# Performance work log

Measured on AMD Instinct MI355X. Metric: run time of the kernel, lower is better.

The kernel has to match this reference:

```python
import jax, jax.numpy as jnp
import numpy as np

NUM_HEADS = 16
INACTIVE = 4          # cfg_comp.attention_heads_inactive
SIG_DIM = 64          # cfg_comp.attention_heads_signature_dim
MLP_HIDDEN = 512      # cfg_comp.attention_heads_inference_mlp_hidden


def setup_inputs() -> dict:
    key = jax.random.key(0)
    ks = jax.random.split(key, 16)
    S, B, E = 2048, 2, 1024
    def xavier(k, shape, gain=1.0):
        fan_in, fan_out = shape[1], shape[0]
        a = gain * np.sqrt(6.0 / (fan_in + fan_out))
        return jax.random.uniform(k, shape, jnp.float32, -a, a)
    g = 1.0 / np.sqrt(2.0)
    return {
        "query": jax.random.normal(ks[0], (S, B, E), jnp.float32),
        "q_w": xavier(ks[1], (E, E), g), "q_b": jnp.zeros((E,), jnp.float32),
        "k_w": xavier(ks[2], (E, E), g), "k_b": jnp.zeros((E,), jnp.float32),
        "v_w": xavier(ks[3], (E, E), g), "v_b": jnp.zeros((E,), jnp.float32),
        "out_w": xavier(ks[4], (E, E)), "out_b": jnp.zeros((E,), jnp.float32),
        "inf1_w": xavier(ks[5], (MLP_HIDDEN, E), np.sqrt(2.0)),
        "inf1_b": jnp.zeros((MLP_HIDDEN,), jnp.float32),
        "inf2_w": xavier(ks[6], (SIG_DIM, MLP_HIDDEN), np.sqrt(2.0)),
        "inf2_b": jnp.zeros((SIG_DIM,), jnp.float32),
        "head_sig": jax.random.normal(ks[7], (NUM_HEADS, SIG_DIM), jnp.float32)
                    * np.sqrt(2.0 / (NUM_HEADS + SIG_DIM)),
    }


def _head_mask(query, inf1_w, inf1_b, inf2_w, inf2_b, head_sig):
    # inference_masking_step: (S, B, E) -> binary mask (B, H, S)
    t = jax.nn.relu(query @ inf1_w.T + inf1_b)          # (S, B, hidden)
    t = t @ inf2_w.T + inf2_b                            # (S, B, sig)
    s = t @ head_sig.T                                   # (S, B, H) head scores
    keep = NUM_HEADS - INACTIVE
    kth = jax.lax.top_k(s, keep)[0][..., -1]             # (S, B) kth-largest score
    mask = (s >= kth[..., None]).astype(query.dtype)     # 1 at top-`keep` heads
    mask = jax.lax.stop_gradient(mask)                   # scatter of constants in torch
    return jnp.transpose(mask, (1, 2, 0))                # (B, H, S)


def reference(query, q_w, q_b, k_w, k_b, v_w, v_b, out_w, out_b,
              inf1_w, inf1_b, inf2_w, inf2_b, head_sig):
    S, B, E = query.shape
    H, D = NUM_HEADS, E // NUM_HEADS
    scaling = D ** (-0.5)

    q = (query @ q_w.T + q_b) * scaling                  # (S, B, E)
    k = query @ k_w.T + k_b
    v = query @ v_w.T + v_b
    # (S, B, E) -> (B, H, S, D)
    to_bhsd = lambda x: jnp.transpose(x.reshape(S, B, H, D), (1, 2, 0, 3))
    q, k, v = to_bhsd(q), to_bhsd(k), to_bhsd(v)

    attn = jax.nn.softmax(jnp.einsum("bhqd,bhkd->bhqk", q, k), axis=-1)
    o = jnp.einsum("bhqk,bhkd->bhqd", attn, v)           # (B, H, S, D)

    mask = _head_mask(query, inf1_w, inf1_b, inf2_w, inf2_b, head_sig)  # (B, H, S)
    o = o * mask[..., None]                              # gate per head per position

    out = jnp.transpose(o, (2, 0, 1, 3)).reshape(S, B, E)
    return out @ out_w.T + out_b
```

## Files before the change

### kernel.cpp

```cpp
#include <hip/hip_runtime.h>
#include <hip/hip_bf16.h>

#define S_LEN 2048
#define BATCH 2
#define EDIM 1024
#define NHEAD 16
#define DHEAD 64
#define HIDDEN 512
#define SIGD 64
#define KEEP 12

typedef __attribute__((ext_vector_type(8))) short bf16x8;
typedef __attribute__((ext_vector_type(4))) float f32x4;

static __device__ __forceinline__ float bf2f(short s) {
  unsigned int u = ((unsigned int)(unsigned short)s) << 16;
  float f; __builtin_memcpy(&f, &u, 4); return f;
}
static __device__ __forceinline__ short f2bf(float f) {
  unsigned int u; __builtin_memcpy(&u, &f, 4);
  u += 0x7fffu + ((u >> 16) & 1u);
  return (short)(u >> 16);
}

#if __has_builtin(__builtin_amdgcn_exp2f)
static __device__ __forceinline__ float fexp2(float x) { return __builtin_amdgcn_exp2f(x); }
#else
static __device__ __forceinline__ float fexp2(float x) { return exp2f(x); }
#endif

static __device__ __forceinline__ void gl_lds16(const short* g, short* l) {
  __builtin_amdgcn_global_load_lds(
      (const __attribute__((address_space(1))) unsigned int*)g,
      (__attribute__((address_space(3))) unsigned int*)l, 16, 0, 0);
}

static __device__ __forceinline__ float bperm_f(int idx, float v) {
  return __builtin_bit_cast(float,
      __builtin_amdgcn_ds_bpermute(idx, __builtin_bit_cast(int, v)));
}

__global__ __launch_bounds__(256) void cvt_all(
    const float* __restrict__ query, const float* __restrict__ inf1_w,
    const float* __restrict__ qw, const float* __restrict__ kw,
    const float* __restrict__ vw, const float* __restrict__ ow,
    short* __restrict__ qh, short* __restrict__ ql,
    short* __restrict__ w1h, short* __restrict__ w1l,
    short* __restrict__ Wq, short* __restrict__ Wk,
    short* __restrict__ Wv, short* __restrict__ Wo)
{
  int blk = blockIdx.x;
  if (blk < 4608) {
    const float* in; short *oh, *ol; int i;
    if (blk < 4096) { in = query;  oh = qh;  ol = ql;  i = (blk * 256 + threadIdx.x) * 4; }
    else            { in = inf1_w; oh = w1h; ol = w1l; i = ((blk - 4096) * 256 + threadIdx.x) * 4; }
    float4 f = *(const float4*)(in + i);
    union { short s[4]; uint2 v; } uh, ul;
    float x[4] = {f.x, f.y, f.z, f.w};
    #pragma unroll
    for (int u = 0; u < 4; ++u) {
      short h = f2bf(x[u]);
      uh.s[u] = h;
      ul.s[u] = f2bf(x[u] - bf2f(h));
    }
    *(uint2*)(oh + i) = uh.v;
    *(uint2*)(ol + i) = ul.v;
  } else {
    int t = blk - 4608;
    int mat = t >> 10, sub = t & 1023;
    const float* in = (mat == 0) ? qw : (mat == 1) ? kw : (mat == 2) ? vw : ow;
    short* out      = (mat == 0) ? Wq : (mat == 1) ? Wk : (mat == 2) ? Wv : Wo;
    int i = (sub * 256 + threadIdx.x) * 4;
    float4 f = *(const float4*)(in + i);
    union { short s[4]; uint2 v; } u;
    u.s[0] = f2bf(f.x); u.s[1] = f2bf(f.y); u.s[2] = f2bf(f.z); u.s[3] = f2bf(f.w);
    *(uint2*)(out + i) = u.v;
  }
}

template<bool F32OUT>
static __device__ __forceinline__ void gemm128_body(
    short* smem,
    const short* __restrict__ A, const short* __restrict__ B,
    const float* __restrict__ bias, void* __restrict__ outv,
    int row0, int col0, float scale)
{
  short* As = smem;
  short* Bs = smem + 128*32;
  const int tid  = threadIdx.x;
  const int wave = tid >> 6, lane = tid & 63;
  const int quad = lane >> 4, l16 = lane & 15;
  const int wr = wave >> 1, wc = wave & 1;
  const int lr = lane >> 2, lc8 = (lane & 3) * 8;

  const short* gA = A + (size_t)(row0 + wave*16 + lr) * EDIM + lc8;
  const short* gB = B + (size_t)(col0 + wave*16 + lr) * EDIM + lc8;
  short* lA = As + wave*512;
  short* lB = Bs + wave*512;

  f32x4 acc[4][4] = {};
  gl_lds16(gA, lA);  gl_lds16(gA + 64*EDIM, lA + 64*32);
  gl_lds16(gB, lB);  gl_lds16(gB + 64*EDIM, lB + 64*32);

  for (int k0 = 0; k0 < EDIM; k0 += 32) {
    __syncthreads();
    bf16x8 af[4], bfr[4];
    #pragma unroll
    for (int i = 0; i < 4; ++i)
      af[i] = *(const bf16x8*)&As[(wr*64 + i*16 + l16)*32 + quad*8];
    #pragma unroll
    for (int j = 0; j < 4; ++j)
      bfr[j] = *(const bf16x8*)&Bs[(wc*64 + j*16 + l16)*32 + quad*8];
    __syncthreads();
    if (k0 + 32 < EDIM) {
      const short* gA2 = gA + k0 + 32;
      const short* gB2 = gB + k0 + 32;
      gl_lds16(gA2, lA);  gl_lds16(gA2 + 64*EDIM, lA + 64*32);
      gl_lds16(gB2, lB);  gl_lds16(gB2 + 64*EDIM, lB + 64*32);
    }
    #pragma unroll
    for (int i = 0; i < 4; ++i)
      #pragma unroll
      for (int j = 0; j < 4; ++j)
        acc[i][j] = __builtin_amdgcn_mfma_f32_16x16x32_bf16(af[i], bfr[j], acc[i][j], 0, 0, 0);
  }
  #pragma unroll
  for (int j = 0; j < 4; ++j) {
    int col = col0 + wc*64 + j*16 + l16;
    float bv = bias[col];
    #pragma unroll
    for (int i = 0; i < 4; ++i) {
      int rowb = row0 + wr*64 + i*16 + quad*4;
      #pragma unroll
      for (int r = 0; r < 4; ++r) {
        float v = (acc[i][j][r] + bv) * scale;
        if constexpr (F32OUT) {
          ((float*)outv)[(size_t)(rowb + r) * EDIM + col] = v;
        } else {
          ((short*)outv)[(size_t)(rowb + r) * EDIM + col] = f2bf(v);
        }
      }
    }
  }
}

static __device__ __forceinline__ void gemm_t1_body(
    short* smem,
    const short* __restrict__ Agh, const short* __restrict__ Agl,
    const short* __restrict__ Bgh, const short* __restrict__ Bgl,
    const float* __restrict__ bias, float* __restrict__ T1,
    int row0, int col0)
{
  short* Ah = smem;
  short* Al = smem + 4096;
  short* Bh = smem + 8192;
  short* Bl = smem + 10240;
  const int tid  = threadIdx.x;
  const int wave = tid >> 6, lane = tid & 63;
  const int quad = lane >> 4, l16 = lane & 15;
  const int wr = wave >> 1, wc = wave & 1;
  const int lr = lane >> 2, lc8 = (lane & 3) * 8;

  const short* gAh = Agh + (size_t)(row0 + wave*16 + lr) * EDIM + lc8;
  const short* gAl = Agl + (size_t)(row0 + wave*16 + lr) * EDIM + lc8;
  const short* gBh = Bgh + (size_t)(col0 + wave*16 + lr) * EDIM + lc8;
  const short* gBl = Bgl + (size_t)(col0 + wave*16 + lr) * EDIM + lc8;
  short* lAh = Ah + wave*512;  short* lAl = Al + wave*512;
  short* lBh = Bh + wave*512;  short* lBl = Bl + wave*512;

  f32x4 acc[4][2] = {};
  gl_lds16(gAh, lAh);  gl_lds16(gAh + 64*EDIM, lAh + 64*32);
  gl_lds16(gAl, lAl);  gl_lds16(gAl + 64*EDIM, lAl + 64*32);
  gl_lds16(gBh, lBh);  gl_lds16(gBl, lBl);

  for (int k0 = 0; k0 < EDIM; k0 += 32) {
    __syncthreads();
    bf16x8 ah[4], al[4], bh[2], bl[2];
    #pragma unroll
    for (int i = 0; i < 4; ++i) {
      ah[i] = *(const bf16x8*)&Ah[(wr*64 + i*16 + l16)*32 + quad*8];
      al[i] = *(const bf16x8*)&Al[(wr*64 + i*16 + l16)*32 + quad*8];
    }
    #pragma unroll
    for (int j = 0; j < 2; ++j) {
      bh[j] = *(const bf16x8*)&Bh[(wc*32 + j*16 + l16)*32 + quad*8];
      bl[j] = *(const bf16x8*)&Bl[(wc*32 + j*16 + l16)*32 + quad*8];
    }
    __syncthreads();
    if (k0 + 32 < EDIM) {
      const short* p;
      p = gAh + k0 + 32;  gl_lds16(p, lAh);  gl_lds16(p + 64*EDIM, lAh + 64*32);
      p = gAl + k0 + 32;  gl_lds16(p, lAl);  gl_lds16(p + 64*EDIM, lAl + 64*32);
      gl_lds16(gBh + k0 + 32, lBh);  gl_lds16(gBl + k0 + 32, lBl);
    }
    #pragma unroll
    for (int i = 0; i < 4; ++i)
      #pragma unroll
      for (int j = 0; j < 2; ++j) {
        acc[i][j] = __builtin_amdgcn_mfma_f32_16x16x32_bf16(ah[i], bh[j], acc[i][j], 0, 0, 0);
        acc[i][j] = __builtin_amdgcn_mfma_f32_16x16x32_bf16(ah[i], bl[j], acc[i][j], 0, 0, 0);
        acc[i][j] = __builtin_amdgcn_mfma_f32_16x16x32_bf16(al[i], bh[j], acc[i][j], 0, 0, 0);
      }
  }
  #pragma unroll
  for (int j = 0; j < 2; ++j) {
    int col = col0 + wc*32 + j*16 + l16;
    float bv = bias[col];
    #pragma unroll
    for (int i = 0; i < 4; ++i) {
      int rowb = row0 + wr*64 + i*16 + quad*4;
      #pragma unroll
      for (int r = 0; r < 4; ++r)
        T1[(size_t)(rowb + r) * HIDDEN + col] = fmaxf(acc[i][j][r] + bv, 0.0f);
    }
  }
}

__global__ __launch_bounds__(256) void mega_gemm1(
    const short* __restrict__ qh, const short* __restrict__ ql,
    const short* __restrict__ w1h, const short* __restrict__ w1l,
    const float* __restrict__ inf1_b, float* __restrict__ T1,
    const short* __restrict__ Wq, const short* __restrict__ Wk,
    const short* __restrict__ Wv,
    const float* __restrict__ qb, const float* __restrict__ kb,
    const float* __restrict__ vb,
    short* __restrict__ Qp, short* __restrict__ Kp, short* __restrict__ Vp)
{
  __shared__ __attribute__((aligned(16))) short smem[12288];
  int blk = blockIdx.x;
  if ((blk & 3) == 3) {
    int id = blk >> 2;
    gemm_t1_body(smem, qh, ql, w1h, w1l, inf1_b, T1,
                 (id & 31) * 128, (id >> 5) * 64);
  } else {
    int id = (blk >> 2) * 3 + (blk & 3);
    int row0 = (id & 31) * 128;
    int rest = id >> 5;
    int mat = rest >> 3, cb = rest & 7;
    const short* B   = (mat == 0) ? Wq : (mat == 1) ? Wk : Wv;
    const float* bia = (mat == 0) ? qb : (mat == 1) ? kb : vb;
    short* out       = (mat == 0) ? Qp : (mat == 1) ? Kp : Vp;
    float scale      = (mat == 0) ? 0.18033688011112042f : 1.0f;
    gemm128_body<false>(smem, qh, B, bia, (void*)out, row0, cb * 128, scale);
  }
}

__global__ __launch_bounds__(256) void mid_kernel(
    const float* __restrict__ T1, const float* __restrict__ inf2_w,
    const float* __restrict__ inf2_b, const float* __restrict__ head_sig,
    float* __restrict__ maskbuf,
    const short* __restrict__ Vp, short* __restrict__ VT)
{
  __shared__ __attribute__((aligned(16))) float fsm[16*HIDDEN + 16*SIGD + 16*NHEAD];
  int blk = blockIdx.x;
  const int tid = threadIdx.x;
  if (blk < 256) {
    float (*t1s)[HIDDEN] = (float(*)[HIDDEN])fsm;
    float (*t2s)[SIGD]   = (float(*)[SIGD])(fsm + 16*HIDDEN);
    float (*ss)[NHEAD]   = (float(*)[NHEAD])(fsm + 16*HIDDEN + 16*SIGD);
    const int tok0 = blk * 16;
    {
      int row = tid >> 4, c0 = (tid & 15) * 32;
      const float* src = T1 + (size_t)(tok0 + row) * HIDDEN + c0;
      #pragma unroll
      for (int u = 0; u < 8; ++u)
        *(float4*)&t1s[row][c0 + u*4] = *(const float4*)(src + u*4);
    }
    __syncthreads();
    #pragma unroll
    for (int it = 0; it < 4; ++it) {
      int idx = tid + it * 256;
      int tok = idx >> 6, j = idx & 63;
      const float4* w4 = (const float4*)(inf2_w + (size_t)j * HIDDEN);
      const float4* t4 = (const float4*)(&t1s[tok][0]);
      float a = inf2_b[j];
      for (int k = 0; k < HIDDEN/4; ++k) {
        float4 wv = w4[k], tv = t4[k];
        a += tv.x*wv.x + tv.y*wv.y + tv.z*wv.z + tv.w*wv.w;
      }
      t2s[tok][j] = a;
    }
    __syncthreads();
    {
      int tok = tid >> 4, h = tid & 15;
      float a = 0.f;
      for (int d = 0; d < SIGD; ++d) a += t2s[tok][d] * head_sig[h*SIGD + d];
      ss[tok][h] = a;
    }
    __syncthreads();
    {
      int tok = tid >> 4, h = tid & 15;
      float sv = ss[tok][h];
      int cnt = 0;
      #pragma unroll
      for (int j = 0; j < NHEAD; ++j) cnt += (ss[tok][j] > sv) ? 1 : 0;
      int gt = tok0 + tok;
      int s = gt >> 1, b = gt & 1;
      maskbuf[((size_t)(b*NHEAD + h)) * S_LEN + s] = (cnt < KEEP) ? 1.0f : 0.0f;
    }
  } else {
    short (*tile)[72] = (short(*)[72])fsm;
    int t = blk - 256;
    const int s0 = (t & 31) * 64, e0 = ((t >> 5) & 15) * 64, b = t >> 9;
    {
      int sr = tid >> 2, ec = (tid & 3) * 16;
      const short* src = Vp + (size_t)(s0 + sr) * 2048 + b * 1024 + e0 + ec;
      *(uint4*)&tile[sr][ec]     = *(const uint4*)src;
      *(uint4*)&tile[sr][ec + 8] = *(const uint4*)(src + 8);
    }
    __syncthreads();
    {
      int er = tid >> 2, sc = (tid & 3) * 16;
      unsigned pack[8];
      #pragma unroll
      for (int u = 0; u < 8; ++u) {
        unsigned lo = (unsigned short)tile[sc + 2*u][er];
        unsigned hi = (unsigned short)tile[sc + 2*u + 1][er];
        pack[u] = lo | (hi << 16);
      }
      short* dst = VT + (size_t)(b * 1024 + e0 + er) * 2048 + s0 + sc;
      *(uint4*)(dst)     = *(uint4*)&pack[0];
      *(uint4*)(dst + 8) = *(uint4*)&pack[4];
    }
  }
}

__global__ __launch_bounds__(256) void flash_attn(
    short* QpOg, const short* __restrict__ Kp, const short* __restrict__ VT,
    const float* __restrict__ maskbuf)
{
  __shared__ __attribute__((aligned(16))) short smem[32768];
  short* KsL = smem;
  short* VtL = smem + 8192;
  short* PsB = smem + 16384;
  short* Qs  = smem + 16384;

  const int bh = blockIdx.x;
  const int b = bh >> 4, h = bh & 15;
  const int q0 = blockIdx.y * 128;
  const int tid = threadIdx.x;
  const int wave = tid >> 6, lane = tid & 63;
  const int quad = lane >> 4, l16 = lane & 15;
  const size_t colbase = (size_t)b * EDIM + h * DHEAD;
  const size_t rstride = (size_t)BATCH * EDIM;
  short* Psw = PsB + wave * 4096;

  const int ix16 = (lane ^ 16) << 2;
  const int ix32 = (lane ^ 32) << 2;

  {
    int row = tid >> 1;
    int cb  = (tid & 1) * 4;
    const short* src = QpOg + (size_t)(q0 + row) * rstride + colbase + cb * 8;
    #pragma unroll
    for (int u = 0; u < 4; ++u) {
      uint4 v = *(const uint4*)(src + u * 8);
      *(uint4*)&Qs[row * 64 + (((cb + u) ^ (row & 7)) * 8)] = v;
    }
  }
  __syncthreads();
  bf16x8 aq[2][2];
  #pragma unroll
  for (int h2 = 0; h2 < 2; ++h2)
    #pragma unroll
    for (int dh = 0; dh < 2; ++dh) {
      int row = wave * 32 + h2 * 16 + l16;
      aq[h2][dh] = *(const bf16x8*)&Qs[row * 64 + (((dh * 4 + quad) ^ (l16 & 7)) * 8)];
    }

  const int kxor = (lane & 7) ^ (lane >> 3);
  const short* gKbase = Kp + colbase + (size_t)(wave * 32 + (lane >> 3)) * rstride + kxor * 8;
  short* ldsK = KsL + wave * 2048;
  const int vrow_l = lane >> 4;
  short* ldsV = VtL + wave * 2048;

  float m_i[2] = {-1e30f, -1e30f};
  float l_i[2] = {0.f, 0.f};
  f32x4 oacc[2][4];
  #pragma unroll
  for (int h2 = 0; h2 < 2; ++h2)
    #pragma unroll
    for (int dt = 0; dt < 4; ++dt) oacc[h2][dt] = f32x4{0.f, 0.f, 0.f, 0.f};

  for (int kv0 = 0; kv0 < S_LEN; kv0 += 128) {
    __syncthreads();
    #pragma unroll
    for (int i = 0; i < 4; ++i) {
      gl_lds16(gKbase + (size_t)(kv0 + i * 8) * rstride, ldsK + i * 512);
      int vrow = wave * 16 + i * 4 + vrow_l;
      int vx = (lane & 15) ^ ((i & 1) * 4 + vrow_l);
      gl_lds16(VT + (size_t)(bh * 64 + vrow) * S_LEN + kv0 + vx * 8, ldsV + i * 512);
    }
    asm volatile("s_waitcnt vmcnt(0)" ::: "memory");
    __syncthreads();

    f32x4 sacc[2][8];
    #pragma unroll
    for (int h2 = 0; h2 < 2; ++h2)
      #pragma unroll
      for (int c = 0; c < 8; ++c) sacc[h2][c] = f32x4{0.f, 0.f, 0.f, 0.f};
    #pragma unroll
    for (int c = 0; c < 8; ++c) {
      const short* kr = &KsL[(c * 16 + l16) * 64];
      bf16x8 k0 = *(const bf16x8*)&kr[((quad     ^ (l16 & 7)) * 8)];
      bf16x8 k1 = *(const bf16x8*)&kr[(((4 + quad) ^ (l16 & 7)) * 8)];
      #pragma unroll
      for (int h2 = 0; h2 < 2; ++h2) {
        sacc[h2][c] = __builtin_amdgcn_mfma_f32_16x16x32_bf16(k0, aq[h2][0], sacc[h2][c], 0, 0, 0);
        sacc[h2][c] = __builtin_amdgcn_mfma_f32_16x16x32_bf16(k1, aq[h2][1], sacc[h2][c], 0, 0, 0);
      }
    }

    #pragma unroll
    for (int h2 = 0; h2 < 2; ++h2) {
      float vm = fmaxf(fmaxf(sacc[h2][0][0], sacc[h2][0][1]),
                       fmaxf(sacc[h2][0][2], sacc[h2][0][3]));
      #pragma unroll
      for (int c = 1; c < 8; ++c)
        vm = fmaxf(vm, fmaxf(fmaxf(sacc[h2][c][0], sacc[h2][c][1]),
                             fmaxf(sacc[h2][c][2], sacc[h2][c][3])));
      vm = fmaxf(vm, bperm_f(ix16, vm));
      vm = fmaxf(vm, bperm_f(ix32, vm));
      float mnew = fmaxf(m_i[h2], vm);
      float alpha = fexp2(m_i[h2] - mnew);
      float rs = 0.f;
      short* pw = Psw + h2 * 2048 + l16 * 128 + (quad & 1) * 4;
      #pragma unroll
      for (int c = 0; c < 8; ++c) {
        float e0 = fexp2(sacc[h2][c][0] - mnew);
        float e1 = fexp2(sacc[h2][c][1] - mnew);
        float e2 = fexp2(sacc[h2][c][2] - mnew);
        float e3 = fexp2(sacc[h2][c][3] - mnew);
        unsigned lo = __builtin_amdgcn_perm(
            __builtin_bit_cast(unsigned, e1),
            __builtin_bit_cast(unsigned, e0), 0x07060302u);
        unsigned hi = __builtin_amdgcn_perm(
            __builtin_bit_cast(unsigned, e3),
            __builtin_bit_cast(unsigned, e2), 0x07060302u);
        int ch = (c * 2 + (quad >> 1)) ^ (l16 & 7);
        uint2 w2; w2.x = lo; w2.y = hi;
        *(uint2*)(pw + ch * 8) = w2;
        rs += (e0 + e1) + (e2 + e3);
      }
      rs += bperm_f(ix16, rs);
      rs += bperm_f(ix32, rs);
      l_i[h2] = l_i[h2] * alpha + rs;
      m_i[h2] = mnew;
      #pragma unroll
      for (int dt = 0; dt < 4; ++dt) {
        oacc[h2][dt][0] *= alpha; oacc[h2][dt][1] *= alpha;
        oacc[h2][dt][2] *= alpha; oacc[h2][dt][3] *= alpha;
      }
    }
    asm volatile("s_waitcnt lgkmcnt(0)" ::: "memory");

    #pragma unroll
    for (int ks = 0; ks < 4; ++ks) {
      const short* pr = Psw + l16 * 128 + (((ks * 4 + quad) ^ (l16 & 7)) * 8);
      bf16x8 ps0 = *(const bf16x8*)pr;
      bf16x8 ps1 = *(const bf16x8*)(pr + 2048);
      #pragma unroll
      for (int dt = 0; dt < 4; ++dt) {
        bf16x8 bb = *(const bf16x8*)&VtL[(dt * 16 + l16) * 128 +
                                         (((ks * 4 + quad) ^ (l16 & 7)) * 8)];
        oacc[0][dt] = __builtin_amdgcn_mfma_f32_16x16x32_bf16(bb, ps0, oacc[0][dt], 0, 0, 0);
        oacc[1][dt] = __builtin_amdgcn_mfma_f32_16x16x32_bf16(bb, ps1, oacc[1][dt], 0, 0, 0);
      }
    }
  }

  #pragma unroll
  for (int h2 = 0; h2 < 2; ++h2) {
    int q = q0 + wave * 32 + h2 * 16 + l16;
    float mk = maskbuf[((size_t)(b * NHEAD + h)) * S_LEN + q];
    float sc = mk / l_i[h2];
    short* dst = QpOg + (size_t)q * rstride + colbase;
    #pragma unroll
    for (int dt = 0; dt < 4; ++dt) {
      #pragma unroll
      for (int p = 0; p < 2; ++p) {
        unsigned lo = (unsigned short)f2bf(oacc[h2][dt][2*p]     * sc);
        unsigned hi = (unsigned short)f2bf(oacc[h2][dt][2*p + 1] * sc);
        *(unsigned*)(dst + dt*16 + quad*4 + 2*p) = lo | (hi << 16);
      }
    }
  }
}

__global__ __launch_bounds__(256) void gemm_out(
    const short* __restrict__ A, const short* __restrict__ W,
    const float* __restrict__ bias, float* __restrict__ out)
{
  __shared__ __attribute__((aligned(16))) short smem[8192];
  gemm128_body<true>(smem, A, W, bias, (void*)out,
                     blockIdx.x * 128, blockIdx.y * 128, 1.0f);
}

extern "C" void kernel_launch(void* const* d_in, const int* in_sizes, int n_in,
                              void* d_out, int out_size, void* d_ws, size_t ws_size,
                              hipStream_t stream)
{
  const float* query   = (const float*)d_in[0];
  const float* q_w     = (const float*)d_in[1];
  const float* q_b     = (const float*)d_in[2];
  const float* k_w     = (const float*)d_in[3];
  const float* k_b     = (const float*)d_in[4];
  const float* v_w     = (const float*)d_in[5];
  const float* v_b     = (const float*)d_in[6];
  const float* out_w   = (const float*)d_in[7];
  const float* out_b   = (const float*)d_in[8];
  const float* inf1_w  = (const float*)d_in[9];
  const float* inf1_b  = (const float*)d_in[10];
  const float* inf2_w  = (const float*)d_in[11];
  const float* inf2_b  = (const float*)d_in[12];
  const float* head_sig= (const float*)d_in[13];

  char* ws = (char*)d_ws;
  short* qh      = (short*)(ws);
  short* VTb     = (short*)(ws);
  short* ql      = (short*)(ws + (size_t)( 8u<<20));
  float* maskbuf = (float*)(ws + (size_t)( 8u<<20));
  short* Qp      = (short*)(ws + (size_t)(16u<<20));
  short* Kp      = (short*)(ws + (size_t)(24u<<20));
  short* Vp      = (short*)(ws + (size_t)(32u<<20));
  short* Wo      = (short*)(ws + (size_t)(40u<<20));
  char* ob = (char*)d_out;
  float* T1  = (float*)(ob);
  short* w1h = (short*)(ob + (size_t)( 8u<<20));
  short* w1l = (short*)(ob + (size_t)( 9u<<20));
  short* Wq  = (short*)(ob + (size_t)(10u<<20));
  short* Wk  = (short*)(ob + (size_t)(12u<<20));
  short* Wv  = (short*)(ob + (size_t)(14u<<20));
  float* out = (float*)d_out;

  dim3 blk(256);
  cvt_all<<<dim3(8704), blk, 0, stream>>>(query, inf1_w, q_w, k_w, v_w, out_w,
                                          qh, ql, w1h, w1l, Wq, Wk, Wv, Wo);
  mega_gemm1<<<dim3(1024), blk, 0, stream>>>(qh, ql, w1h, w1l, inf1_b, T1,
                                             Wq, Wk, Wv, q_b, k_b, v_b, Qp, Kp, Vp);
  mid_kernel<<<dim3(1280), blk, 0, stream>>>(T1, inf2_w, inf2_b, head_sig, maskbuf,
                                             Vp, VTb);
  flash_attn<<<dim3(32, 16), blk, 0, stream>>>(Qp, Kp, VTb, maskbuf);
  gemm_out<<<dim3(32, 8), blk, 0, stream>>>(Qp, Wo, out_b, out);
}
```

Baseline: 309.8 us.

## Shrink output GEMM tile, interleave mask and V-transpose blocks, add occupancy hint

The output projection gets its own kernel with 128x64 tiles, doubling the grid from 256 to 512 blocks so more of the GPU's compute units are busy. The mask-inference part of mid_kernel now handles 8 tokens per block, with each thread computing two outputs, and its blocks are interleaved with the V-transpose blocks (one in three). This is meant to balance load across the grid. mega_gemm1 gets a launch_bounds hint asking for 4 blocks per CU, which may constrain register allocation.

```diff
diff --git a/kernel.cpp b/kernel.cpp
--- a/kernel.cpp
+++ b/kernel.cpp
@@ -78,11 +78,10 @@
   }
 }
 
-template<bool F32OUT>
 static __device__ __forceinline__ void gemm128_body(
     short* smem,
     const short* __restrict__ A, const short* __restrict__ B,
-    const float* __restrict__ bias, void* __restrict__ outv,
+    const float* __restrict__ bias, short* __restrict__ outv,
     int row0, int col0, float scale)
 {
   short* As = smem;
@@ -134,11 +133,7 @@
       #pragma unroll
       for (int r = 0; r < 4; ++r) {
         float v = (acc[i][j][r] + bv) * scale;
-        if constexpr (F32OUT) {
-          ((float*)outv)[(size_t)(rowb + r) * EDIM + col] = v;
-        } else {
-          ((short*)outv)[(size_t)(rowb + r) * EDIM + col] = f2bf(v);
-        }
+        outv[(size_t)(rowb + r) * EDIM + col] = f2bf(v);
       }
     }
   }
@@ -216,7 +211,7 @@
   }
 }
 
-__global__ __launch_bounds__(256) void mega_gemm1(
+__global__ __launch_bounds__(256, 4) void mega_gemm1(
     const short* __restrict__ qh, const short* __restrict__ ql,
     const short* __restrict__ w1h, const short* __restrict__ w1l,
     const float* __restrict__ inf1_b, float* __restrict__ T1,
@@ -241,7 +236,7 @@
     const float* bia = (mat == 0) ? qb : (mat == 1) ? kb : vb;
     short* out       = (mat == 0) ? Qp : (mat == 1) ? Kp : Vp;
     float scale      = (mat == 0) ? 0.18033688011112042f : 1.0f;
-    gemm128_body<false>(smem, qh, B, bia, (void*)out, row0, cb * 128, scale);
+    gemm128_body(smem, qh, B, bia, out, row0, cb * 128, scale);
   }
 }
 
@@ -251,44 +246,46 @@
     float* __restrict__ maskbuf,
     const short* __restrict__ Vp, short* __restrict__ VT)
 {
-  __shared__ __attribute__((aligned(16))) float fsm[16*HIDDEN + 16*SIGD + 16*NHEAD];
+  __shared__ __attribute__((aligned(16))) float fsm[8*HIDDEN + 8*SIGD + 8*NHEAD];
   int blk = blockIdx.x;
+  const int g = blk / 3, r3 = blk % 3;
   const int tid = threadIdx.x;
-  if (blk < 256) {
+  if (r3 == 2) {
     float (*t1s)[HIDDEN] = (float(*)[HIDDEN])fsm;
-    float (*t2s)[SIGD]   = (float(*)[SIGD])(fsm + 16*HIDDEN);
-    float (*ss)[NHEAD]   = (float(*)[NHEAD])(fsm + 16*HIDDEN + 16*SIGD);
-    const int tok0 = blk * 16;
+    float (*t2s)[SIGD]   = (float(*)[SIGD])(fsm + 8*HIDDEN);
+    float (*ss)[NHEAD]   = (float(*)[NHEAD])(fsm + 8*HIDDEN + 8*SIGD);
+    const int tok0 = g * 8;
     {
-      int row = tid >> 4, c0 = (tid & 15) * 32;
+      int row = tid >> 5, c0 = (tid & 31) * 16;
       const float* src = T1 + (size_t)(tok0 + row) * HIDDEN + c0;
       #pragma unroll
-      for (int u = 0; u < 8; ++u)
+      for (int u = 0; u < 4; ++u)
         *(float4*)&t1s[row][c0 + u*4] = *(const float4*)(src + u*4);
     }
     __syncthreads();
-    #pragma unroll
-    for (int it = 0; it < 4; ++it) {
-      int idx = tid + it * 256;
-      int tok = idx >> 6, j = idx & 63;
-      const float4* w4 = (const float4*)(inf2_w + (size_t)j * HIDDEN);
+    {
+      int tok = tid >> 5, j0 = (tid & 31) * 2;
+      const float4* w0 = (const float4*)(inf2_w + (size_t)j0 * HIDDEN);
+      const float4* w1 = (const float4*)(inf2_w + (size_t)(j0 + 1) * HIDDEN);
       const float4* t4 = (const float4*)(&t1s[tok][0]);
-      float a = inf2_b[j];
+      float a0 = inf2_b[j0], a1 = inf2_b[j0 + 1];
       for (int k = 0; k < HIDDEN/4; ++k) {
-        float4 wv = w4[k], tv = t4[k];
-        a += tv.x*wv.x + tv.y*wv.y + tv.z*wv.z + tv.w*wv.w;
-      }
-      t2s[tok][j] = a;
-    }
-    __syncthreads();
-    {
+        float4 tv = t4[k];
+        float4 v0 = w0[k], v1 = w1[k];
+        a0 += tv.x*v0.x + tv.y*v0.y + tv.z*v0.z + tv.w*v0.w;
+        a1 += tv.x*v1.x + tv.y*v1.y + tv.z*v1.z + tv.w*v1.w;
+      }
+      t2s[tok][j0] = a0; t2s[tok][j0 + 1] = a1;
+    }
+    __syncthreads();
+    if (tid < 128) {
       int tok = tid >> 4, h = tid & 15;
       float a = 0.f;
       for (int d = 0; d < SIGD; ++d) a += t2s[tok][d] * head_sig[h*SIGD + d];
       ss[tok][h] = a;
     }
     __syncthreads();
-    {
+    if (tid < 128) {
       int tok = tid >> 4, h = tid & 15;
       float sv = ss[tok][h];
       int cnt = 0;
@@ -300,7 +297,7 @@
     }
   } else {
     short (*tile)[72] = (short(*)[72])fsm;
-    int t = blk - 256;
+    int t = g * 2 + r3;
     const int s0 = (t & 31) * 64, e0 = ((t >> 5) & 15) * 64, b = t >> 9;
     {
       int sr = tid >> 2, ec = (tid & 3) * 16;
@@ -491,9 +488,58 @@
     const short* __restrict__ A, const short* __restrict__ W,
     const float* __restrict__ bias, float* __restrict__ out)
 {
-  __shared__ __attribute__((aligned(16))) short smem[8192];
-  gemm128_body<true>(smem, A, W, bias, (void*)out,
-                     blockIdx.x * 128, blockIdx.y * 128, 1.0f);
+  __shared__ __attribute__((aligned(16))) short smem[6144];
+  short* As = smem;
+  short* Bs = smem + 4096;
+  const int tid  = threadIdx.x;
+  const int wave = tid >> 6, lane = tid & 63;
+  const int quad = lane >> 4, l16 = lane & 15;
+  const int wr = wave >> 1, wc = wave & 1;
+  const int lr = lane >> 2, lc8 = (lane & 3) * 8;
+  const int row0 = blockIdx.x * 128, col0 = blockIdx.y * 64;
+
+  const short* gA = A + (size_t)(row0 + wave*16 + lr) * EDIM + lc8;
+  const short* gB = W + (size_t)(col0 + wave*16 + lr) * EDIM + lc8;
+  short* lA = As + wave*512;
+  short* lB = Bs + wave*512;
+
+  f32x4 acc[4][2] = {};
+  gl_lds16(gA, lA);  gl_lds16(gA + 64*EDIM, lA + 64*32);
+  gl_lds16(gB, lB);
+
+  for (int k0 = 0; k0 < EDIM; k0 += 32) {
+    __syncthreads();
+    bf16x8 af[4], bfr[2];
+    #pragma unroll
+    for (int i = 0; i < 4; ++i)
+      af[i] = *(const bf16x8*)&As[(wr*64 + i*16 + l16)*32 + quad*8];
+    #pragma unroll
+    for (int j = 0; j < 2; ++j)
+      bfr[j] = *(const bf16x8*)&Bs[(wc*32 + j*16 + l16)*32 + quad*8];
+    __syncthreads();
+    if (k0 + 32 < EDIM) {
+      const short* gA2 = gA + k0 + 32;
+      gl_lds16(gA2, lA);  gl_lds16(gA2 + 64*EDIM, lA + 64*32);
+      gl_lds16(gB + k0 + 32, lB);
+    }
+    #pragma unroll
+    for (int i = 0; i < 4; ++i)
+      #pragma unroll
+      for (int j = 0; j < 2; ++j)
+        acc[i][j] = __builtin_amdgcn_mfma_f32_16x16x32_bf16(af[i], bfr[j], acc[i][j], 0, 0, 0);
+  }
+  #pragma unroll
+  for (int j = 0; j < 2; ++j) {
+    int col = col0 + wc*32 + j*16 + l16;
+    float bv = bias[col];
+    #pragma unroll
+    for (int i = 0; i < 4; ++i) {
+      int rowb = row0 + wr*64 + i*16 + quad*4;
+      #pragma unroll
+      for (int r = 0; r < 4; ++r)
+        out[(size_t)(rowb + r) * EDIM + col] = acc[i][j][r] + bv;
+    }
+  }
 }
 
 extern "C" void kernel_launch(void* const* d_in, const int* in_sizes, int n_in,
@@ -538,8 +584,8 @@
                                           qh, ql, w1h, w1l, Wq, Wk, Wv, Wo);
   mega_gemm1<<<dim3(1024), blk, 0, stream>>>(qh, ql, w1h, w1l, inf1_b, T1,
                                              Wq, Wk, Wv, q_b, k_b, v_b, Qp, Kp, Vp);
-  mid_kernel<<<dim3(1280), blk, 0, stream>>>(T1, inf2_w, inf2_b, head_sig, maskbuf,
+  mid_kernel<<<dim3(1536), blk, 0, stream>>>(T1, inf2_w, inf2_b, head_sig, maskbuf,
                                              Vp, VTb);
   flash_attn<<<dim3(32, 16), blk, 0, stream>>>(Qp, Kp, VTb, maskbuf);
-  gemm_out<<<dim3(32, 8), blk, 0, stream>>>(Qp, Wo, out_b, out);
-}
+  gemm_out<<<dim3(32, 16), blk, 0, stream>>>(Qp, Wo, out_b, out);
+}
```

After: 302.8 us. -2.3%, faster.
